# Optimization experiments

Measured on AMD Instinct MI355X. Metric: run time of the kernel, lower is better.

The kernel has to match this reference:

```python
import jax, jax.numpy as jnp
import numpy as np


def conv1x1(x, w, b):
    # x: [B,Cin,H,W], w: [Cout,Cin], b: [Cout]
    return jnp.einsum('bchw,oc->bohw', x, w) + b[None, :, None, None]


def _lin_idx_w(in_size, out_size):
    # PyTorch bilinear, align_corners=False: src = max((i+0.5)*scale - 0.5, 0)
    scale = in_size / out_size
    src = jnp.maximum((jnp.arange(out_size, dtype=jnp.float32) + 0.5) * scale - 0.5, 0.0)
    i0 = jnp.floor(src).astype(jnp.int32)
    i0 = jnp.minimum(i0, in_size - 1)
    i1 = jnp.minimum(i0 + 1, in_size - 1)
    w1 = src - i0.astype(jnp.float32)
    return i0, i1, w1


def bilinear_resize(x, out_h, out_w):
    Hin, Win = x.shape[-2], x.shape[-1]
    y0, y1, wy = _lin_idx_w(Hin, out_h)
    x0, x1, wx = _lin_idx_w(Win, out_w)
    wy = wy[:, None]  # [out_h,1]
    rows = x[:, :, y0, :] * (1.0 - wy) + x[:, :, y1, :] * wy
    out = rows[:, :, :, x0] * (1.0 - wx) + rows[:, :, :, x1] * wx      # [B,C,out_h,out_w]
    return out


def setup_inputs() -> dict:
    key = jax.random.key(0)
    ks = jax.random.split(key, 10)
    C, C8 = 512, 64
    s = 1.0 / np.sqrt(C)
    return {
        'content': jax.random.normal(ks[0], (4, C, 64, 64), jnp.float32),
        'style': jax.random.normal(ks[1], (4, C, 80, 80), jnp.float32),
        'f_w': jax.random.normal(ks[2], (C8, C), jnp.float32) * s,
        'f_b': jax.random.normal(ks[3], (C8,), jnp.float32) * 0.01,
        'g_w': jax.random.normal(ks[4], (C8, C), jnp.float32) * s,
        'g_b': jax.random.normal(ks[5], (C8,), jnp.float32) * 0.01,
        'h_w': jax.random.normal(ks[6], (C, C), jnp.float32) * s,
        'h_b': jax.random.normal(ks[7], (C,), jnp.float32) * 0.01,
        'out_w': jax.random.normal(ks[8], (C, C), jnp.float32) * s,
        'out_b': jax.random.normal(ks[9], (C,), jnp.float32) * 0.01,
    }


def reference(content, style, f_w, f_b, g_w, g_b, h_w, h_b, out_w, out_b):
    B, C, H, W = content.shape
    HW = H * W
    f = conv1x1(content, f_w, f_b).reshape(B, -1, HW)                       # [B,C8,HW] (query, pre-transpose)
    g = bilinear_resize(conv1x1(style, g_w, g_b), H, W).reshape(B, -1, HW)  # [B,C8,HW]
    h = bilinear_resize(conv1x1(style, h_w, h_b), H, W).reshape(B, C, HW)   # [B,C,HW]
    attn = jax.nn.softmax(jnp.einsum('bcm,bcn->bmn', f, g), axis=-1)        # [B,HW_q,HW_k]
    out = jnp.einsum('bcn,bmn->bcm', h, attn).reshape(B, C, H, W)
    return conv1x1(out, out_w, out_b)
```

## Files before the change

### kernel.cpp

```cpp
#include <hip/hip_runtime.h>

#define NB 4
#define NC 512
#define ND 64
#define HW 4096
#define SPIN 6400

typedef _Float16 f16;
typedef _Float16 f16x8 __attribute__((ext_vector_type(8)));
typedef short s16x8 __attribute__((ext_vector_type(8)));
typedef short s16x4 __attribute__((ext_vector_type(4)));
typedef float f32x4 __attribute__((ext_vector_type(4)));
typedef float f32x16 __attribute__((ext_vector_type(16)));
typedef unsigned short ushortT;

__device__ __forceinline__ unsigned short f32_to_bf16(float x) {
  union { float f; unsigned u; } v; v.f = x;
  unsigned r = v.u + 0x7FFFu + ((v.u >> 16) & 1u);
  return (unsigned short)(r >> 16);
}

__device__ __forceinline__ void stv(float* p, float v) { *p = v; }
__device__ __forceinline__ void stv(f16* p, float v) { *p = (f16)v; }
__device__ __forceinline__ void stv(unsigned short* p, float v) { *p = f32_to_bf16(v); }

__device__ __forceinline__ unsigned cvt_pk_bf16(float lo, float hi) {
  unsigned r;
  asm("v_cvt_pk_bf16_f32 %0, %1, %2" : "=v"(r) : "v"(lo), "v"(hi));
  return r;
}

__global__ __launch_bounds__(256) void cvtw_kernel(const float* __restrict__ fw,
                                                   const float* __restrict__ gw,
                                                   const float* __restrict__ hw,
                                                   const float* __restrict__ ow,
                                                   f16* __restrict__ dst) {
  int i = blockIdx.x * 256 + threadIdx.x;
  const float* src; int off;
  if (i < 32768) { src = fw; off = 0; }
  else if (i < 65536) { src = gw; off = 32768; }
  else if (i < 327680) { src = hw; off = 65536; }
  else { src = ow; off = 327680; }
  dst[i] = (f16)src[i - off];
}

__global__ __launch_bounds__(256) void tcvt_kernel(const float* __restrict__ in,
                                                   f16* __restrict__ out) {
  __shared__ float Xs[64][65];
  int p0 = blockIdx.x * 64, c0 = blockIdx.y * 64, b = blockIdx.z;
  int t = threadIdx.x;
  const float* ib = in + ((size_t)b * NC + c0) * HW + p0;
  int pl = t & 63, cg = t >> 6;
#pragma unroll
  for (int k = 0; k < 16; ++k) {
    int c = cg * 16 + k;
    Xs[c][pl] = ib[(size_t)c * HW + pl];
  }
  __syncthreads();
  int p = t >> 2, cb = (t & 3) * 16;
  union { f16 h[16]; float4 q[2]; } u;
#pragma unroll
  for (int j = 0; j < 16; ++j) u.h[j] = (f16)Xs[cb + j][p];
  f16* ob = out + ((size_t)b * HW + p0 + p) * NC + c0 + cb;
  *(float4*)(ob) = u.q[0];
  *(float4*)(ob + 8) = u.q[1];
}

__global__ __launch_bounds__(256) void rstcvt_kernel(const float* __restrict__ X,
                                                     f16* __restrict__ Y) {
  __shared__ float Xs[64 * 165];
  int oy = blockIdx.x, c0 = blockIdx.y * 64, b = blockIdx.z;
  float syf = fmaxf((oy + 0.5f) * 1.25f - 0.5f, 0.f);
  int y0 = (int)syf; int y1 = min(y0 + 1, 79); float wy = syf - (float)y0;
  int t = threadIdx.x;
  const float* Xb = X + ((size_t)b * NC + c0) * SPIN;
#pragma unroll
  for (int k = 0; k < 10; ++k) {
    int idx = t + k * 256;
    int c = idx / 40;
    int rem = idx - c * 40;
    int yy = rem / 20;
    int x4 = rem - yy * 20;
    int ysrc = yy ? y1 : y0;
    float4 v = *(const float4*)(Xb + (size_t)c * SPIN + ysrc * 80 + x4 * 4);
    float* d = Xs + c * 165 + yy * 82 + x4 * 4;
    d[0] = v.x; d[1] = v.y; d[2] = v.z; d[3] = v.w;
  }
  __syncthreads();
  int ox = t >> 2, cb = (t & 3) * 16;
  float sxf = fmaxf((ox + 0.5f) * 1.25f - 0.5f, 0.f);
  int x0 = (int)sxf; int x1 = min(x0 + 1, 79); float wx = sxf - (float)x0;
  union { f16 h[16]; float4 q[2]; } u;
#pragma unroll
  for (int j = 0; j < 16; ++j) {
    const float* base = Xs + (cb + j) * 165;
    float a0 = base[x0], a1 = base[x1];
    float b0 = base[82 + x0], b1 = base[82 + x1];
    float r0 = a0 + (a1 - a0) * wx;
    float r1 = b0 + (b1 - b0) * wx;
    u.h[j] = (f16)(r0 + (r1 - r0) * wy);
  }
  f16* ob = Y + ((size_t)b * HW + oy * 64 + ox) * NC + c0 + cb;
  *(float4*)(ob) = u.q[0];
  *(float4*)(ob + 8) = u.q[1];
}

__global__ __launch_bounds__(256) void convpm2_kernel(const f16* __restrict__ X0,
                                                      const f16* __restrict__ X1,
                                                      const f16* __restrict__ W01,
                                                      const float* __restrict__ b0,
                                                      const float* __restrict__ b1,
                                                      f16* __restrict__ Y0,
                                                      f16* __restrict__ Y1) {
  int sel = blockIdx.z >> 2;
  int b = blockIdx.z & 3;
  const f16* X = sel ? X1 : X0;
  const f16* W = W01 + sel * (ND * NC);
  const float* bias = sel ? b1 : b0;
  f16* Y = sel ? Y1 : Y0;
  int t = threadIdx.x, l = t & 63, w = t >> 6;
  int pw = blockIdx.x * 256 + w * 64;
  int l4 = l & 15, g = l >> 4;
  f32x4 acc[4][4] = {};
  const f16* Xb = X + ((size_t)b * HW + pw) * NC;
  for (int kk = 0; kk < 16; ++kk) {
    int co = kk * 32 + g * 8;
    f16x8 a[4], bb[4];
#pragma unroll
    for (int ms = 0; ms < 4; ++ms) a[ms] = *(const f16x8*)(Xb + (size_t)(ms * 16 + l4) * NC + co);
#pragma unroll
    for (int ct = 0; ct < 4; ++ct) bb[ct] = *(const f16x8*)(W + (size_t)(ct * 16 + l4) * NC + co);
#pragma unroll
    for (int ms = 0; ms < 4; ++ms)
#pragma unroll
      for (int ct = 0; ct < 4; ++ct)
        acc[ms][ct] = __builtin_amdgcn_mfma_f32_16x16x32_f16(a[ms], bb[ct], acc[ms][ct], 0, 0, 0);
  }
  float bv[4];
#pragma unroll
  for (int ct = 0; ct < 4; ++ct) bv[ct] = bias[ct * 16 + l4];
  f16* Yb = Y + ((size_t)b * HW + pw) * ND;
#pragma unroll
  for (int ms = 0; ms < 4; ++ms)
#pragma unroll
    for (int ct = 0; ct < 4; ++ct)
#pragma unroll
      for (int r = 0; r < 4; ++r)
        Yb[(size_t)(ms * 16 + g * 4 + r) * ND + ct * 16 + l4] = (f16)(acc[ms][ct][r] + bv[ct]);
}

template <typename OUT_T>
__global__ __launch_bounds__(256) void convcm_kernel(const f16* __restrict__ X,
                                                     const f16* __restrict__ W,
                                                     const float* __restrict__ bias,
                                                     OUT_T* __restrict__ Y, int O) {
  int b = blockIdx.z;
  int o0 = blockIdx.x * 64;
  int t = threadIdx.x, l = t & 63, w = t >> 6;
  int pw = blockIdx.y * 256 + w * 64;
  int l4 = l & 15, g = l >> 4;
  f32x4 acc[4][4] = {};
  const f16* Xb = X + ((size_t)b * HW + pw) * NC;
  const f16* Wb = W + (size_t)o0 * NC;
  for (int kk = 0; kk < 16; ++kk) {
    int co = kk * 32 + g * 8;
    f16x8 a[4], bb[4];
#pragma unroll
    for (int ms = 0; ms < 4; ++ms) a[ms] = *(const f16x8*)(Wb + (size_t)(ms * 16 + l4) * NC + co);
#pragma unroll
    for (int ct = 0; ct < 4; ++ct) bb[ct] = *(const f16x8*)(Xb + (size_t)(ct * 16 + l4) * NC + co);
#pragma unroll
    for (int ms = 0; ms < 4; ++ms)
#pragma unroll
      for (int ct = 0; ct < 4; ++ct)
        acc[ms][ct] = __builtin_amdgcn_mfma_f32_16x16x32_f16(a[ms], bb[ct], acc[ms][ct], 0, 0, 0);
  }
  float bv[4][4];
#pragma unroll
  for (int ms = 0; ms < 4; ++ms)
#pragma unroll
    for (int r = 0; r < 4; ++r) bv[ms][r] = bias[o0 + ms * 16 + g * 4 + r];
#pragma unroll
  for (int ms = 0; ms < 4; ++ms)
#pragma unroll
    for (int ct = 0; ct < 4; ++ct)
#pragma unroll
      for (int r = 0; r < 4; ++r) {
        float val = acc[ms][ct][r] + bv[ms][r];
        stv(&Y[((size_t)b * O + o0 + ms * 16 + g * 4 + r) * HW + pw + ct * 16 + l4], val);
      }
}

union PAu { unsigned u[4]; s16x8 v; };
union VSu { s16x8 v; s16x4 h[2]; };

__global__ __launch_bounds__(256, 2) void attn_kernel(const f16* __restrict__ FT,
                                                      const f16* __restrict__ GT,
                                                      const unsigned short* __restrict__ HC,
                                                      f16* __restrict__ MIDT) {
  __shared__ __align__(16) char Vs[2][32768];
  int bid = blockIdx.x;
  int b = (bid & 7) >> 1;
  int cs = bid & 1;
  int mt = bid >> 3;
  int t = threadIdx.x, l = t & 63, w = t >> 6;
  int lm = l & 31, hf = l >> 5;
  int mf = w >> 1, cq = w & 1;
  int mr = mt * 64 + mf * 32;
  int cqb = cq * 128;

  const f16* Fq = FT + ((size_t)b * HW + mr + lm) * ND + hf * 8;
  f16x8 q[4];
#pragma unroll
  for (int kc = 0; kc < 4; ++kc) q[kc] = *(const f16x8*)(Fq + kc * 16);

  const f16* kp = GT + (size_t)b * HW * ND + (size_t)lm * ND + hf * 8;

  int sc = t >> 3;
  int nseg = (t & 7) * 8;
  int sb0 = ((nseg >> 4) * 32) + (((nseg >> 3) & 1) * 8);
  const unsigned short* vsrc =
      HC + ((size_t)b * NC + cs * 256 + sc) * HW + nseg;

  f32x16 acc[4] = {};
  float den = 0.f;

#define STAGE_LOAD(n0x)                                                   \
  do {                                                                    \
    _Pragma("unroll") for (int r_ = 0; r_ < 8; ++r_)                      \
        vreg[r_].v = *(const s16x8*)(vsrc + (size_t)r_ * 32 * HW + (n0x)); \
  } while (0)

#define STAGE_WRITE(bufidx)                                               \
  do {                                                                    \
    _Pragma("unroll") for (int r_ = 0; r_ < 8; ++r_) {                    \
      int cl_ = r_ * 32 + sc;                                             \
      char* row_ = Vs[bufidx] + cl_ * 128;                                \
      int sw_ = (cl_ & 7) << 4;                                           \
      *(s16x4*)(row_ + (sb0 ^ sw_)) = vreg[r_].h[0];                      \
      *(s16x4*)(row_ + ((sb0 + 16) ^ sw_)) = vreg[r_].h[1];               \
    }                                                                     \
  } while (0)

#define PACK(sv, o)                                                       \
  do {                                                                    \
    float p_[16];                                                         \
    _Pragma("unroll") for (int r_ = 0; r_ < 16; ++r_) {                   \
      p_[r_] = __expf(sv[r_]);                                            \
      den += p_[r_];                                                      \
    }                                                                     \
    pa[o].u[0] = cvt_pk_bf16(p_[0], p_[1]);                               \
    pa[o].u[1] = cvt_pk_bf16(p_[2], p_[3]);                               \
    pa[o].u[2] = cvt_pk_bf16(p_[4], p_[5]);                               \
    pa[o].u[3] = cvt_pk_bf16(p_[6], p_[7]);                               \
    pa[o + 1].u[0] = cvt_pk_bf16(p_[8], p_[9]);                           \
    pa[o + 1].u[1] = cvt_pk_bf16(p_[10], p_[11]);                         \
    pa[o + 1].u[2] = cvt_pk_bf16(p_[12], p_[13]);                         \
    pa[o + 1].u[3] = cvt_pk_bf16(p_[14], p_[15]);                         \
  } while (0)

  {
    VSu vreg[8];
    STAGE_LOAD(0);
    STAGE_WRITE(0);
  }
  __syncthreads();

  f16x8 kbA[4], kbB[4];
#pragma unroll
  for (int kc = 0; kc < 4; ++kc) kbA[kc] = *(const f16x8*)(kp + kc * 16);

  const int cl0 = cqb + lm;
  const int vsw = (lm & 7) << 4;

  int cur = 0;
  for (int it = 0; it < 64; ++it) {
    const int n0 = it * 64;
    VSu vreg[8];
    if (it < 63) STAGE_LOAD(n0 + 64);
#pragma unroll
    for (int kc = 0; kc < 4; ++kc)
      kbB[kc] = *(const f16x8*)(kp + (size_t)(n0 + 32) * ND + kc * 16);
    PAu pa[4];
    {
      f32x16 s = {};
#pragma unroll
      for (int kc = 0; kc < 4; ++kc)
        s = __builtin_amdgcn_mfma_f32_32x32x16_f16(kbA[kc], q[kc], s, 0, 0, 0);
      PACK(s, 0);
    }
    if (it < 63) {
#pragma unroll
      for (int kc = 0; kc < 4; ++kc)
        kbA[kc] = *(const f16x8*)(kp + (size_t)(n0 + 64) * ND + kc * 16);
    }
    {
      f32x16 s = {};
#pragma unroll
      for (int kc = 0; kc < 4; ++kc)
        s = __builtin_amdgcn_mfma_f32_32x32x16_f16(kbB[kc], q[kc], s, 0, 0, 0);
      PACK(s, 2);
    }
    const char* Vc = Vs[cur];
    s16x8 vb[4], vn[4];
#pragma unroll
    for (int kn = 0; kn < 4; ++kn)
      vb[kn] = *(const s16x8*)(Vc + cl0 * 128 + ((kn * 32 + hf * 16) ^ vsw));
#pragma unroll
    for (int cf = 0; cf < 4; ++cf) {
      if (cf < 3) {
        const char* vr = Vc + (cl0 + (cf + 1) * 32) * 128;
#pragma unroll
        for (int kn = 0; kn < 4; ++kn)
          vn[kn] = *(const s16x8*)(vr + ((kn * 32 + hf * 16) ^ vsw));
      }
      __builtin_amdgcn_s_setprio(1);
#pragma unroll
      for (int kn = 0; kn < 4; ++kn)
        acc[cf] = __builtin_amdgcn_mfma_f32_32x32x16_bf16(pa[kn].v, vb[kn], acc[cf], 0, 0, 0);
      __builtin_amdgcn_s_setprio(0);
      if (cf < 3) {
#pragma unroll
        for (int kn = 0; kn < 4; ++kn) vb[kn] = vn[kn];
      }
    }
    if (it < 63) STAGE_WRITE(cur ^ 1);
    __syncthreads();
    cur ^= 1;
  }
#undef STAGE_LOAD
#undef STAGE_WRITE
#undef PACK

  den += __shfl_xor(den, 32);
  float rd = 1.f / den;
  f16* Mb = MIDT + ((size_t)b * HW + mr) * NC + cs * 256 + cqb + lm;
#pragma unroll
  for (int r = 0; r < 16; ++r) {
    int mrow = (r & 3) + 8 * (r >> 2) + 4 * hf;
    float rv = __shfl(rd, mrow);
#pragma unroll
    for (int cf = 0; cf < 4; ++cf)
      Mb[(size_t)mrow * NC + cf * 32] = (f16)(acc[cf][r] * rv);
  }
}

extern "C" void kernel_launch(void* const* d_in, const int* in_sizes, int n_in,
                              void* d_out, int out_size, void* d_ws, size_t ws_size,
                              hipStream_t stream) {
  const float* content = (const float*)d_in[0];
  const float* style   = (const float*)d_in[1];
  const float* f_w = (const float*)d_in[2];
  const float* f_b = (const float*)d_in[3];
  const float* g_w = (const float*)d_in[4];
  const float* g_b = (const float*)d_in[5];
  const float* h_w = (const float*)d_in[6];
  const float* h_b = (const float*)d_in[7];
  const float* out_w = (const float*)d_in[8];
  const float* out_b = (const float*)d_in[9];
  float* out = (float*)d_out;

  const size_t MB = 1ull << 20;
  char* base = (char*)d_ws;
  f16* contentT = (f16*)base;
  f16* midT     = (f16*)base;
  unsigned short* hC = (unsigned short*)(base + 16 * MB);
  f16* fT = (f16*)(base + 32 * MB);
  f16* gT = (f16*)(base + 34 * MB);
  f16* styrT = (f16*)(base + 48 * MB);
  f16* w16 = (f16*)(base + 64 * MB);
  f16* fw16 = w16;
  f16* gw16 = w16 + 32768;
  f16* hw16 = w16 + 65536;
  f16* ow16 = w16 + 327680;

  cvtw_kernel<<<dim3(589824 / 256), 256, 0, stream>>>(f_w, g_w, h_w, out_w, w16);
  tcvt_kernel<<<dim3(HW / 64, NC / 64, NB), 256, 0, stream>>>(content, contentT);
  rstcvt_kernel<<<dim3(64, NC / 64, NB), 256, 0, stream>>>(style, styrT);
  convpm2_kernel<<<dim3(HW / 256, 1, 2 * NB), 256, 0, stream>>>(contentT, styrT, fw16, f_b, g_b, fT, gT);
  convcm_kernel<unsigned short><<<dim3(NC / 64, HW / 256, NB), 256, 0, stream>>>(styrT, hw16, h_b, hC, NC);
  attn_kernel<<<dim3(512), 256, 0, stream>>>(fT, gT, hC, midT);
  convcm_kernel<float><<<dim3(NC / 64, HW / 256, NB), 256, 0, stream>>>(midT, ow16, out_b, out, NC);
}
```

Measured before the change: 280.7 us.

## Software-pipeline attention loop so PV MFMAs of previous tile overlap QK and exp

Restructures the main key loop into a two-stage software pipeline. Each step issues the QK^T MFMAs for the current key tile, then runs the P·V MFMAs for the previous tile, then does the exp/bf16 packing of the current scores. It ping-pongs two sets of probability and key-fragment registers, with a manual unroll by two and a prologue and epilogue. The aim is to hide exp/convert latency and the QK-to-PV dependency behind matrix-core work. The cost is higher register pressure from the doubled fragment buffers, which could lower occupancy or cause spills.

```diff
diff --git a/kernel.cpp b/kernel.cpp
--- a/kernel.cpp
+++ b/kernel.cpp
@@ -225,6 +225,9 @@
   f32x16 acc[4] = {};
   float den = 0.f;
 
+  const int cl0 = cqb + lm;
+  const int vsw = (lm & 7) << 4;
+
 #define STAGE_LOAD(n0x)                                                   \
   do {                                                                    \
     _Pragma("unroll") for (int r_ = 0; r_ < 8; ++r_)                      \
@@ -242,21 +245,67 @@
     }                                                                     \
   } while (0)
 
-#define PACK(sv, o)                                                       \
+#define PACK(sv, PA, o)                                                   \
   do {                                                                    \
     float p_[16];                                                         \
     _Pragma("unroll") for (int r_ = 0; r_ < 16; ++r_) {                   \
       p_[r_] = __expf(sv[r_]);                                            \
       den += p_[r_];                                                      \
     }                                                                     \
-    pa[o].u[0] = cvt_pk_bf16(p_[0], p_[1]);                               \
-    pa[o].u[1] = cvt_pk_bf16(p_[2], p_[3]);                               \
-    pa[o].u[2] = cvt_pk_bf16(p_[4], p_[5]);                               \
-    pa[o].u[3] = cvt_pk_bf16(p_[6], p_[7]);                               \
-    pa[o + 1].u[0] = cvt_pk_bf16(p_[8], p_[9]);                           \
-    pa[o + 1].u[1] = cvt_pk_bf16(p_[10], p_[11]);                         \
-    pa[o + 1].u[2] = cvt_pk_bf16(p_[12], p_[13]);                         \
-    pa[o + 1].u[3] = cvt_pk_bf16(p_[14], p_[15]);                         \
+    PA[o].u[0] = cvt_pk_bf16(p_[0], p_[1]);                               \
+    PA[o].u[1] = cvt_pk_bf16(p_[2], p_[3]);                               \
+    PA[o].u[2] = cvt_pk_bf16(p_[4], p_[5]);                               \
+    PA[o].u[3] = cvt_pk_bf16(p_[6], p_[7]);                               \
+    PA[o + 1].u[0] = cvt_pk_bf16(p_[8], p_[9]);                           \
+    PA[o + 1].u[1] = cvt_pk_bf16(p_[10], p_[11]);                         \
+    PA[o + 1].u[2] = cvt_pk_bf16(p_[12], p_[13]);                         \
+    PA[o + 1].u[3] = cvt_pk_bf16(p_[14], p_[15]);                         \
+  } while (0)
+
+#define PVBODY(PA, Vc)                                                    \
+  do {                                                                    \
+    s16x8 vb_[4], vn_[4];                                                 \
+    _Pragma("unroll") for (int kn = 0; kn < 4; ++kn)                      \
+        vb_[kn] = *(const s16x8*)((Vc) + cl0 * 128 + ((kn * 32 + hf * 16) ^ vsw)); \
+    _Pragma("unroll") for (int cf = 0; cf < 4; ++cf) {                    \
+      if (cf < 3) {                                                       \
+        const char* vr_ = (Vc) + (cl0 + (cf + 1) * 32) * 128;             \
+        _Pragma("unroll") for (int kn = 0; kn < 4; ++kn)                  \
+            vn_[kn] = *(const s16x8*)(vr_ + ((kn * 32 + hf * 16) ^ vsw)); \
+      }                                                                   \
+      __builtin_amdgcn_s_setprio(1);                                      \
+      _Pragma("unroll") for (int kn = 0; kn < 4; ++kn)                    \
+          acc[cf] = __builtin_amdgcn_mfma_f32_32x32x16_bf16(PA[kn].v, vb_[kn], acc[cf], 0, 0, 0); \
+      __builtin_amdgcn_s_setprio(0);                                      \
+      if (cf < 3) {                                                       \
+        _Pragma("unroll") for (int kn = 0; kn < 4; ++kn) vb_[kn] = vn_[kn]; \
+      }                                                                   \
+    }                                                                     \
+  } while (0)
+
+#define ITER(IT, PC, PP, KC, KN, DOPV)                                    \
+  do {                                                                    \
+    const int n0 = (IT) * 64;                                             \
+    VSu vreg[8];                                                          \
+    if ((IT) < 63) {                                                      \
+      STAGE_LOAD(n0 + 64);                                                \
+      _Pragma("unroll") for (int h_ = 0; h_ < 2; ++h_)                    \
+          _Pragma("unroll") for (int kc = 0; kc < 4; ++kc)                \
+          KN[h_][kc] = *(const f16x8*)(kp + (size_t)(n0 + 64 + h_ * 32) * ND + kc * 16); \
+    }                                                                     \
+    f32x16 s0 = {}, s1 = {};                                              \
+    _Pragma("unroll") for (int kc = 0; kc < 4; ++kc)                      \
+        s0 = __builtin_amdgcn_mfma_f32_32x32x16_f16(KC[0][kc], q[kc], s0, 0, 0, 0); \
+    _Pragma("unroll") for (int kc = 0; kc < 4; ++kc)                      \
+        s1 = __builtin_amdgcn_mfma_f32_32x32x16_f16(KC[1][kc], q[kc], s1, 0, 0, 0); \
+    if (DOPV) {                                                           \
+      const char* Vc_ = Vs[((IT) + 1) & 1];              \
+      PVBODY(PP, Vc_);                                                    \
+    }                                                                     \
+    PACK(s0, PC, 0);                                                      \
+    PACK(s1, PC, 2);                                                      \
+    __syncthreads();                                                      \
+    if ((IT) < 63) STAGE_WRITE(((IT) + 1) & 1);                           \
   } while (0)
 
   {
@@ -264,73 +313,28 @@
     STAGE_LOAD(0);
     STAGE_WRITE(0);
   }
+  f16x8 kbP[2][4], kbQ[2][4];
+#pragma unroll
+  for (int h = 0; h < 2; ++h)
+#pragma unroll
+    for (int kc = 0; kc < 4; ++kc)
+      kbP[h][kc] = *(const f16x8*)(kp + (size_t)(h * 32) * ND + kc * 16);
   __syncthreads();
 
-  f16x8 kbA[4], kbB[4];
-#pragma unroll
-  for (int kc = 0; kc < 4; ++kc) kbA[kc] = *(const f16x8*)(kp + kc * 16);
-
-  const int cl0 = cqb + lm;
-  const int vsw = (lm & 7) << 4;
-
-  int cur = 0;
-  for (int it = 0; it < 64; ++it) {
-    const int n0 = it * 64;
-    VSu vreg[8];
-    if (it < 63) STAGE_LOAD(n0 + 64);
-#pragma unroll
-    for (int kc = 0; kc < 4; ++kc)
-      kbB[kc] = *(const f16x8*)(kp + (size_t)(n0 + 32) * ND + kc * 16);
-    PAu pa[4];
-    {
-      f32x16 s = {};
-#pragma unroll
-      for (int kc = 0; kc < 4; ++kc)
-        s = __builtin_amdgcn_mfma_f32_32x32x16_f16(kbA[kc], q[kc], s, 0, 0, 0);
-      PACK(s, 0);
-    }
-    if (it < 63) {
-#pragma unroll
-      for (int kc = 0; kc < 4; ++kc)
-        kbA[kc] = *(const f16x8*)(kp + (size_t)(n0 + 64) * ND + kc * 16);
-    }
-    {
-      f32x16 s = {};
-#pragma unroll
-      for (int kc = 0; kc < 4; ++kc)
-        s = __builtin_amdgcn_mfma_f32_32x32x16_f16(kbB[kc], q[kc], s, 0, 0, 0);
-      PACK(s, 2);
-    }
-    const char* Vc = Vs[cur];
-    s16x8 vb[4], vn[4];
-#pragma unroll
-    for (int kn = 0; kn < 4; ++kn)
-      vb[kn] = *(const s16x8*)(Vc + cl0 * 128 + ((kn * 32 + hf * 16) ^ vsw));
-#pragma unroll
-    for (int cf = 0; cf < 4; ++cf) {
-      if (cf < 3) {
-        const char* vr = Vc + (cl0 + (cf + 1) * 32) * 128;
-#pragma unroll
-        for (int kn = 0; kn < 4; ++kn)
-          vn[kn] = *(const s16x8*)(vr + ((kn * 32 + hf * 16) ^ vsw));
-      }
-      __builtin_amdgcn_s_setprio(1);
-#pragma unroll
-      for (int kn = 0; kn < 4; ++kn)
-        acc[cf] = __builtin_amdgcn_mfma_f32_32x32x16_bf16(pa[kn].v, vb[kn], acc[cf], 0, 0, 0);
-      __builtin_amdgcn_s_setprio(0);
-      if (cf < 3) {
-#pragma unroll
-        for (int kn = 0; kn < 4; ++kn) vb[kn] = vn[kn];
-      }
-    }
-    if (it < 63) STAGE_WRITE(cur ^ 1);
-    __syncthreads();
-    cur ^= 1;
-  }
+  PAu paA[4], paB[4];
+  ITER(0, paA, paB, kbP, kbQ, false);
+  for (int ito = 1; ito < 63; ito += 2) {
+    ITER(ito, paB, paA, kbQ, kbP, true);
+    ITER(ito + 1, paA, paB, kbP, kbQ, true);
+  }
+  ITER(63, paB, paA, kbQ, kbP, true);
+  PVBODY(paB, (const char*)Vs[1]);
+
 #undef STAGE_LOAD
 #undef STAGE_WRITE
 #undef PACK
+#undef PVBODY
+#undef ITER
 
   den += __shfl_xor(den, 32);
   float rd = 1.f / den;
```

Result: no change. 276.4 us (-1.5%).
